# Optimization experiments

Hardware: AMD Instinct MI355X
Metric: run time of the kernel (lower is better)

Reference implementation:

```python
import jax, jax.numpy as jnp
import numpy as np
import math

B, S, D = 4, 2048, 1024


def setup_inputs() -> dict:
    key = jax.random.key(0)
    k1, k2, k3 = jax.random.split(key, 3)
    X = jax.random.normal(k1, (B, S, D), dtype=jnp.float32)
    # causal mask, broadcast over batch (True = keep)
    mask = jnp.broadcast_to(jnp.tril(jnp.ones((S, S), dtype=bool)), (B, S, S))
    # torch nn.Linear weights: y = x @ W.T; init scale ~ 1/sqrt(D)
    WQK = jax.random.normal(k2, (D, D), dtype=jnp.float32) / math.sqrt(D)
    WOV = jax.random.normal(k3, (D, D), dtype=jnp.float32) / math.sqrt(D)
    return {"X": X, "mask": mask, "WQK": WQK, "WOV": WOV}


def reference(X, mask, WQK, WOV):
    d = X.shape[-1]
    Q = jnp.einsum('bsd,ed->bse', X, WQK)          # WQK(X) = X @ WQK.T
    Sc = jnp.einsum('bse,bte->bst', Q, X)          # shared-QK scores: Q @ X^T
    # NOTE: original multiplies by sqrt(d_model) (not divide) - faithful
    Sc = Sc * jnp.asarray(math.sqrt(d), Sc.dtype)
    Sc = jnp.where(mask, Sc, -jnp.inf)
    A = jax.nn.softmax(Sc, axis=-1)                # dropout p=0.0 -> identity
    V = jnp.einsum('bsd,ed->bse', X, WOV)          # WOV(X)
    Y = jnp.einsum('bst,bte->bse', A, V)
    return (X + Y, A)
```

## Files before the change

### kernel.cpp

```cpp
#include <hip/hip_runtime.h>
#include <hip/hip_fp16.h>
#include <math.h>

typedef _Float16 half_t;
typedef _Float16 h8_t __attribute__((ext_vector_type(8)));
typedef _Float16 h4_t __attribute__((ext_vector_type(4)));
typedef float f4_t __attribute__((ext_vector_type(4)));

#define MFMA16(a, b, c) __builtin_amdgcn_mfma_f32_16x16x32_f16(a, b, c, 0, 0, 0)

static constexpr int kB = 4;
static constexpr int kS = 2048;
static constexpr int kD = 1024;
static constexpr int BM = 128;
static constexpr int BN = 128;
static constexpr int BK = 32;

__device__ __forceinline__ void gload16(const half_t* g, half_t* l) {
  __builtin_amdgcn_global_load_lds(
      (const __attribute__((address_space(1))) void*)g,
      (__attribute__((address_space(3))) void*)l, 16, 0, 0);
}

__device__ __forceinline__ void stage_tile(half_t* __restrict__ sm,
                                           const half_t* __restrict__ g, int ld) {
  const int t = threadIdx.x;
  const int r = t >> 2;
  const int c = (t & 3) * 8;
  gload16(&g[(size_t)r * ld + c], &sm[r * BK + c]);
  gload16(&g[(size_t)(r + 64) * ld + c], &sm[(r + 64) * BK + c]);
}

template <bool SPLIT>
__device__ __forceinline__ void stage_all(half_t* buf, const half_t* Ahi,
                                          const half_t* Alo, int lda,
                                          const half_t* Bhi, const half_t* Blo,
                                          int ldb, size_t ko) {
  stage_tile(buf, Ahi + ko, lda);
  stage_tile(buf + BM * BK, Bhi + ko, ldb);
  if (SPLIT) {
    stage_tile(buf + 2 * BM * BK, Alo + ko, lda);
    stage_tile(buf + 3 * BM * BK, Blo + ko, ldb);
  }
}

template <bool SPLIT>
__device__ __forceinline__ void gemm_core(const half_t* __restrict__ Ahi,
                                          const half_t* __restrict__ Alo, int lda,
                                          const half_t* __restrict__ Bhi,
                                          const half_t* __restrict__ Blo, int ldb,
                                          int k_iters, half_t* sm, f4_t acc[4][4]) {
  constexpr int BUFSZ = (SPLIT ? 4 : 2) * BM * BK;
  const int lane = threadIdx.x & 63;
  const int wid = threadIdx.x >> 6;
  const int wm = (wid >> 1) * 64;
  const int wn = (wid & 1) * 64;
  const int fr = lane & 15;
  const int fk = (lane >> 4) * 8;

  half_t* cur = sm;
  half_t* nxt = sm + BUFSZ;

  stage_all<SPLIT>(cur, Ahi, Alo, lda, Bhi, Blo, ldb, 0);
  asm volatile("s_waitcnt vmcnt(0)" ::: "memory");
  __builtin_amdgcn_s_barrier();

  for (int kk = 0; kk < k_iters; ++kk) {
    if (kk + 1 < k_iters)
      stage_all<SPLIT>(nxt, Ahi, Alo, lda, Bhi, Blo, ldb, (size_t)(kk + 1) * BK);
    const half_t* sAh = cur;
    const half_t* sBh = cur + BM * BK;
    const half_t* sAl = cur + 2 * BM * BK;
    const half_t* sBl = cur + 3 * BM * BK;
    h8_t a[4], b[4], al[4], bl[4];
#pragma unroll
    for (int i = 0; i < 4; ++i) {
      a[i] = *(const h8_t*)&sAh[(wm + i * 16 + fr) * BK + fk];
      b[i] = *(const h8_t*)&sBh[(wn + i * 16 + fr) * BK + fk];
      if (SPLIT) {
        al[i] = *(const h8_t*)&sAl[(wm + i * 16 + fr) * BK + fk];
        bl[i] = *(const h8_t*)&sBl[(wn + i * 16 + fr) * BK + fk];
      }
    }
#pragma unroll
    for (int i = 0; i < 4; ++i)
#pragma unroll
      for (int j = 0; j < 4; ++j) {
        acc[i][j] = MFMA16(a[i], b[j], acc[i][j]);
        if (SPLIT) {
          acc[i][j] = MFMA16(a[i], bl[j], acc[i][j]);
          acc[i][j] = MFMA16(al[i], b[j], acc[i][j]);
        }
      }
    asm volatile("s_waitcnt vmcnt(0)" ::: "memory");
    __builtin_amdgcn_s_barrier();
    half_t* t = cur; cur = nxt; nxt = t;
  }
}

__global__ __launch_bounds__(256) void gemm_q_kernel(
    const half_t* __restrict__ Xhi, const half_t* __restrict__ Xlo,
    const half_t* __restrict__ Whi, const half_t* __restrict__ Wlo,
    half_t* __restrict__ Qhi, half_t* __restrict__ Qlo) {
  __shared__ half_t sm[2 * 4 * BM * BK];
  const size_t arow = (size_t)blockIdx.y * BM;
  const size_t brow = (size_t)blockIdx.x * BN;
  f4_t acc[4][4] = {};
  gemm_core<true>(Xhi + arow * kD, Xlo + arow * kD, kD,
                  Whi + brow * kD, Wlo + brow * kD, kD, kD / BK, sm, acc);
  const int lane = threadIdx.x & 63;
  const int wid = threadIdx.x >> 6;
  const int wm = (wid >> 1) * 64, wn = (wid & 1) * 64;
  const int c16 = lane & 15, r4 = (lane >> 4) * 4;
#pragma unroll
  for (int i = 0; i < 4; ++i)
#pragma unroll
    for (int j = 0; j < 4; ++j)
#pragma unroll
      for (int r = 0; r < 4; ++r) {
        const size_t row = arow + wm + i * 16 + r4 + r;
        const size_t col = brow + wn + j * 16 + c16;
        const float q = acc[i][j][r];
        const half_t qh = (half_t)q;
        const half_t ql = (half_t)(q - (float)qh);
        const size_t idx = row * kD + col;
        Qhi[idx] = qh;
        Qlo[idx] = ql;
      }
}

__global__ __launch_bounds__(256) void gemm_v_kernel(
    const half_t* __restrict__ Xhi, const half_t* __restrict__ Whi,
    half_t* __restrict__ Vt) {
  __shared__ half_t sm[2 * 2 * BM * BK];
  const size_t arow = (size_t)blockIdx.y * BM;
  const size_t brow = (size_t)blockIdx.x * BN;
  f4_t acc[4][4] = {};
  gemm_core<false>(Xhi + arow * kD, nullptr, kD, Whi + brow * kD, nullptr, kD,
                   kD / BK, sm, acc);
  const int lane = threadIdx.x & 63;
  const int wid = threadIdx.x >> 6;
  const int wm = (wid >> 1) * 64, wn = (wid & 1) * 64;
  const int c16 = lane & 15, r4 = (lane >> 4) * 4;
#pragma unroll
  for (int i = 0; i < 4; ++i)
#pragma unroll
    for (int j = 0; j < 4; ++j)
#pragma unroll
      for (int r = 0; r < 4; ++r) {
        const size_t row = arow + wm + i * 16 + r4 + r;
        const size_t col = brow + wn + j * 16 + c16;
        const size_t bi = row >> 11;
        const size_t s = row & 2047;
        Vt[bi * (size_t)kD * kS + col * kS + s] = (half_t)acc[i][j][r];
      }
}

__global__ __launch_bounds__(256) void gemm_score_kernel(
    const half_t* __restrict__ Qhi, const half_t* __restrict__ Qlo,
    const half_t* __restrict__ Xhi, const half_t* __restrict__ Xlo,
    float* __restrict__ Sc) {
  const int tn = blockIdx.x, tm = blockIdx.y, bi = blockIdx.z;
  if (tn > tm) return;
  __shared__ half_t sm[2 * 4 * BM * BK];
  const size_t arow = (size_t)bi * kS + (size_t)tm * BM;
  const size_t brow = (size_t)bi * kS + (size_t)tn * BN;
  f4_t acc[4][4] = {};
  gemm_core<true>(Qhi + arow * kD, Qlo + arow * kD, kD,
                  Xhi + brow * kD, Xlo + brow * kD, kD, kD / BK, sm, acc);
  float* out = Sc + (size_t)bi * kS * kS;
  const int lane = threadIdx.x & 63;
  const int wid = threadIdx.x >> 6;
  const int wm = (wid >> 1) * 64, wn = (wid & 1) * 64;
  const int c16 = lane & 15, r4 = (lane >> 4) * 4;
#pragma unroll
  for (int i = 0; i < 4; ++i)
#pragma unroll
    for (int j = 0; j < 4; ++j)
#pragma unroll
      for (int r = 0; r < 4; ++r) {
        const int row = tm * BM + wm + i * 16 + r4 + r;
        const int col = tn * BN + wn + j * 16 + c16;
        out[(size_t)row * kS + col] = 32.0f * acc[i][j][r];
      }
}

__global__ __launch_bounds__(256) void softmax_kernel(float* __restrict__ A,
                                                      half_t* __restrict__ Ah) {
  const int rgl = blockIdx.x;
  const int s = rgl & 2047;
  float* row = A + (size_t)rgl * kS;
  half_t* hrow = Ah + (size_t)rgl * kS;
  const int tid = threadIdx.x;
  const int n = s + 1;
  float v[8];
  float mx = -INFINITY;
#pragma unroll
  for (int i = 0; i < 8; ++i) {
    const int t = tid + i * 256;
    v[i] = (t < n) ? row[t] : -INFINITY;
    mx = fmaxf(mx, v[i]);
  }
  for (int off = 32; off; off >>= 1) mx = fmaxf(mx, __shfl_xor(mx, off));
  __shared__ float red[8];
  const int lane = tid & 63, wid = tid >> 6;
  if (lane == 0) red[wid] = mx;
  __syncthreads();
  if (tid == 0) {
    float m = fmaxf(fmaxf(red[0], red[1]), fmaxf(red[2], red[3]));
    red[4] = m;
  }
  __syncthreads();
  mx = red[4];
  float sum = 0.0f;
#pragma unroll
  for (int i = 0; i < 8; ++i) {
    v[i] = (tid + i * 256 < n) ? __expf(v[i] - mx) : 0.0f;
    sum += v[i];
  }
  for (int off = 32; off; off >>= 1) sum += __shfl_xor(sum, off);
  __syncthreads();
  if (lane == 0) red[wid] = sum;
  __syncthreads();
  if (tid == 0) red[5] = 1.0f / (red[0] + red[1] + red[2] + red[3]);
  __syncthreads();
  const float inv = red[5];
#pragma unroll
  for (int i = 0; i < 8; ++i) {
    const int t = tid + i * 256;
    const float a = v[i] * inv;
    row[t] = a;
    hrow[t] = (half_t)a;
  }
}

__global__ __launch_bounds__(256) void gemm_y_kernel(
    const half_t* __restrict__ Ah, const half_t* __restrict__ Vt,
    const float* __restrict__ X, float* __restrict__ Out) {
  __shared__ half_t sm[2 * 2 * BM * BK];
  const int tn = blockIdx.x, bi = blockIdx.z;
  const int tm = (kS / BM - 1) - blockIdx.y;
  const size_t abase = ((size_t)bi * kS + (size_t)tm * BM) * kS;
  const size_t bbase = ((size_t)bi * kD + (size_t)tn * BN) * kS;
  f4_t acc[4][4] = {};
  gemm_core<false>(Ah + abase, nullptr, kS, Vt + bbase, nullptr, kS,
                   (tm + 1) * BM / BK, sm, acc);
  const size_t obase = (size_t)bi * kS * kD;
  const int lane = threadIdx.x & 63;
  const int wid = threadIdx.x >> 6;
  const int wm = (wid >> 1) * 64, wn = (wid & 1) * 64;
  const int c16 = lane & 15, r4 = (lane >> 4) * 4;
#pragma unroll
  for (int i = 0; i < 4; ++i)
#pragma unroll
    for (int j = 0; j < 4; ++j)
#pragma unroll
      for (int r = 0; r < 4; ++r) {
        const size_t row = (size_t)tm * BM + wm + i * 16 + r4 + r;
        const size_t col = (size_t)tn * BN + wn + j * 16 + c16;
        const size_t idx = obase + row * kD + col;
        Out[idx] = X[idx] + acc[i][j][r];
      }
}

__global__ __launch_bounds__(256) void split_kernel(const float* __restrict__ x,
                                                    half_t* __restrict__ hi,
                                                    half_t* __restrict__ lo, int n4) {
  const int i = blockIdx.x * 256 + threadIdx.x;
  if (i >= n4) return;
  const float4 v = ((const float4*)x)[i];
  const float vv[4] = {v.x, v.y, v.z, v.w};
  h4_t h, l;
#pragma unroll
  for (int j = 0; j < 4; ++j) {
    const half_t hh = (half_t)vv[j];
    h[j] = hh;
    l[j] = (half_t)(vv[j] - (float)hh);
  }
  ((h4_t*)hi)[i] = h;
  ((h4_t*)lo)[i] = l;
}

__global__ __launch_bounds__(256) void cvt_kernel(const float* __restrict__ x,
                                                  half_t* __restrict__ hi, int n4) {
  const int i = blockIdx.x * 256 + threadIdx.x;
  if (i >= n4) return;
  const float4 v = ((const float4*)x)[i];
  h4_t h;
  h[0] = (half_t)v.x; h[1] = (half_t)v.y; h[2] = (half_t)v.z; h[3] = (half_t)v.w;
  ((h4_t*)hi)[i] = h;
}

extern "C" void kernel_launch(void* const* d_in, const int* in_sizes, int n_in,
                              void* d_out, int out_size, void* d_ws, size_t ws_size,
                              hipStream_t stream) {
  const float* X   = (const float*)d_in[0];
  const float* WQK = (const float*)d_in[2];
  const float* WOV = (const float*)d_in[3];

  constexpr size_t nX = (size_t)kB * kS * kD;
  constexpr size_t nW = (size_t)kD * kD;
  constexpr size_t nA = (size_t)kB * kS * kS;

  float* out0 = (float*)d_out;
  float* outA = out0 + nX;

  half_t* ws = (half_t*)d_ws;
  half_t* Xhi = ws; ws += nX;
  half_t* Xlo = ws; ws += nX;
  half_t* Qhi = ws; ws += nX;
  half_t* Qlo = ws; ws += nX;
  half_t* Whi = ws; ws += nW;
  half_t* Wlo = ws; ws += nW;
  half_t* WVh = ws; ws += nW;
  half_t* Vt  = ws; ws += nX;
  half_t* Ah  = ws; ws += nA;
  const size_t need_bytes = (size_t)((char*)ws - (char*)d_ws);
  if (ws_size < need_bytes) return;

  split_kernel<<<(int)(nX / 4 / 256), 256, 0, stream>>>(X, Xhi, Xlo, (int)(nX / 4));
  split_kernel<<<(int)(nW / 4 / 256), 256, 0, stream>>>(WQK, Whi, Wlo, (int)(nW / 4));
  cvt_kernel<<<(int)(nW / 4 / 256), 256, 0, stream>>>(WOV, WVh, (int)(nW / 4));

  gemm_q_kernel<<<dim3(kD / BN, kB * kS / BM), 256, 0, stream>>>(Xhi, Xlo, Whi, Wlo, Qhi, Qlo);
  gemm_v_kernel<<<dim3(kD / BN, kB * kS / BM), 256, 0, stream>>>(Xhi, WVh, Vt);
  gemm_score_kernel<<<dim3(kS / BN, kS / BM, kB), 256, 0, stream>>>(Qhi, Qlo, Xhi, Xlo, outA);
  softmax_kernel<<<kB * kS, 256, 0, stream>>>(outA, Ah);
  gemm_y_kernel<<<dim3(kD / BN, kS / BM, kB), 256, 0, stream>>>(Ah, Vt, X, out0);
}
```

Before: 391.5 us.

## Use 512-thread blocks with 8 waves and XOR-swizzled LDS tiles in GEMMs

Doubles the GEMM block size to 512 threads (8 waves arranged 2x4, each computing a 64x32 sub-tile) so each wave holds half as many accumulators, and each thread stages one 16-byte chunk per tile instead of two. It also applies an XOR swizzle on the k-column of global loads and on the fragment reads, intended to reduce LDS bank conflicts. The aim is more waves in flight to hide latency, at the cost of less register-level reuse per wave and more LDS traffic per MFMA.

```diff
diff --git a/kernel.cpp b/kernel.cpp
--- a/kernel.cpp
+++ b/kernel.cpp
@@ -15,6 +15,7 @@
 static constexpr int BM = 128;
 static constexpr int BN = 128;
 static constexpr int BK = 32;
+static constexpr int NT = 512;
 
 __device__ __forceinline__ void gload16(const half_t* g, half_t* l) {
   __builtin_amdgcn_global_load_lds(
@@ -26,9 +27,8 @@
                                            const half_t* __restrict__ g, int ld) {
   const int t = threadIdx.x;
   const int r = t >> 2;
-  const int c = (t & 3) * 8;
-  gload16(&g[(size_t)r * ld + c], &sm[r * BK + c]);
-  gload16(&g[(size_t)(r + 64) * ld + c], &sm[(r + 64) * BK + c]);
+  const int c = ((t & 3) * 8) ^ ((((r >> 1) & 3)) << 3);
+  gload16(&g[(size_t)r * ld + c], &sm[r * BK + (t & 3) * 8]);
 }
 
 template <bool SPLIT>
@@ -49,14 +49,14 @@
                                           const half_t* __restrict__ Alo, int lda,
                                           const half_t* __restrict__ Bhi,
                                           const half_t* __restrict__ Blo, int ldb,
-                                          int k_iters, half_t* sm, f4_t acc[4][4]) {
+                                          int k_iters, half_t* sm, f4_t acc[4][2]) {
   constexpr int BUFSZ = (SPLIT ? 4 : 2) * BM * BK;
   const int lane = threadIdx.x & 63;
   const int wid = threadIdx.x >> 6;
-  const int wm = (wid >> 1) * 64;
-  const int wn = (wid & 1) * 64;
+  const int wm = (wid >> 2) * 64;
+  const int wn = (wid & 3) * 32;
   const int fr = lane & 15;
-  const int fk = (lane >> 4) * 8;
+  const int fk = (((lane >> 4) * 8) ^ (((lane >> 1) & 3) << 3));
 
   half_t* cur = sm;
   half_t* nxt = sm + BUFSZ;
@@ -72,20 +72,21 @@
     const half_t* sBh = cur + BM * BK;
     const half_t* sAl = cur + 2 * BM * BK;
     const half_t* sBl = cur + 3 * BM * BK;
-    h8_t a[4], b[4], al[4], bl[4];
+    h8_t a[4], b[2], al[4], bl[2];
 #pragma unroll
     for (int i = 0; i < 4; ++i) {
       a[i] = *(const h8_t*)&sAh[(wm + i * 16 + fr) * BK + fk];
-      b[i] = *(const h8_t*)&sBh[(wn + i * 16 + fr) * BK + fk];
-      if (SPLIT) {
-        al[i] = *(const h8_t*)&sAl[(wm + i * 16 + fr) * BK + fk];
-        bl[i] = *(const h8_t*)&sBl[(wn + i * 16 + fr) * BK + fk];
-      }
+      if (SPLIT) al[i] = *(const h8_t*)&sAl[(wm + i * 16 + fr) * BK + fk];
     }
 #pragma unroll
+    for (int j = 0; j < 2; ++j) {
+      b[j] = *(const h8_t*)&sBh[(wn + j * 16 + fr) * BK + fk];
+      if (SPLIT) bl[j] = *(const h8_t*)&sBl[(wn + j * 16 + fr) * BK + fk];
+    }
+#pragma unroll
     for (int i = 0; i < 4; ++i)
 #pragma unroll
-      for (int j = 0; j < 4; ++j) {
+      for (int j = 0; j < 2; ++j) {
         acc[i][j] = MFMA16(a[i], b[j], acc[i][j]);
         if (SPLIT) {
           acc[i][j] = MFMA16(a[i], bl[j], acc[i][j]);
@@ -98,24 +99,24 @@
   }
 }
 
-__global__ __launch_bounds__(256) void gemm_q_kernel(
+__global__ __launch_bounds__(NT) void gemm_q_kernel(
     const half_t* __restrict__ Xhi, const half_t* __restrict__ Xlo,
     const half_t* __restrict__ Whi, const half_t* __restrict__ Wlo,
     half_t* __restrict__ Qhi, half_t* __restrict__ Qlo) {
   __shared__ half_t sm[2 * 4 * BM * BK];
   const size_t arow = (size_t)blockIdx.y * BM;
   const size_t brow = (size_t)blockIdx.x * BN;
-  f4_t acc[4][4] = {};
+  f4_t acc[4][2] = {};
   gemm_core<true>(Xhi + arow * kD, Xlo + arow * kD, kD,
                   Whi + brow * kD, Wlo + brow * kD, kD, kD / BK, sm, acc);
   const int lane = threadIdx.x & 63;
   const int wid = threadIdx.x >> 6;
-  const int wm = (wid >> 1) * 64, wn = (wid & 1) * 64;
+  const int wm = (wid >> 2) * 64, wn = (wid & 3) * 32;
   const int c16 = lane & 15, r4 = (lane >> 4) * 4;
 #pragma unroll
   for (int i = 0; i < 4; ++i)
 #pragma unroll
-    for (int j = 0; j < 4; ++j)
+    for (int j = 0; j < 2; ++j)
 #pragma unroll
       for (int r = 0; r < 4; ++r) {
         const size_t row = arow + wm + i * 16 + r4 + r;
@@ -129,23 +130,23 @@
       }
 }
 
-__global__ __launch_bounds__(256) void gemm_v_kernel(
+__global__ __launch_bounds__(NT) void gemm_v_kernel(
     const half_t* __restrict__ Xhi, const half_t* __restrict__ Whi,
     half_t* __restrict__ Vt) {
   __shared__ half_t sm[2 * 2 * BM * BK];
   const size_t arow = (size_t)blockIdx.y * BM;
   const size_t brow = (size_t)blockIdx.x * BN;
-  f4_t acc[4][4] = {};
+  f4_t acc[4][2] = {};
   gemm_core<false>(Xhi + arow * kD, nullptr, kD, Whi + brow * kD, nullptr, kD,
                    kD / BK, sm, acc);
   const int lane = threadIdx.x & 63;
   const int wid = threadIdx.x >> 6;
-  const int wm = (wid >> 1) * 64, wn = (wid & 1) * 64;
+  const int wm = (wid >> 2) * 64, wn = (wid & 3) * 32;
   const int c16 = lane & 15, r4 = (lane >> 4) * 4;
 #pragma unroll
   for (int i = 0; i < 4; ++i)
 #pragma unroll
-    for (int j = 0; j < 4; ++j)
+    for (int j = 0; j < 2; ++j)
 #pragma unroll
       for (int r = 0; r < 4; ++r) {
         const size_t row = arow + wm + i * 16 + r4 + r;
@@ -156,7 +157,7 @@
       }
 }
 
-__global__ __launch_bounds__(256) void gemm_score_kernel(
+__global__ __launch_bounds__(NT) void gemm_score_kernel(
     const half_t* __restrict__ Qhi, const half_t* __restrict__ Qlo,
     const half_t* __restrict__ Xhi, const half_t* __restrict__ Xlo,
     float* __restrict__ Sc) {
@@ -165,18 +166,18 @@
   __shared__ half_t sm[2 * 4 * BM * BK];
   const size_t arow = (size_t)bi * kS + (size_t)tm * BM;
   const size_t brow = (size_t)bi * kS + (size_t)tn * BN;
-  f4_t acc[4][4] = {};
+  f4_t acc[4][2] = {};
   gemm_core<true>(Qhi + arow * kD, Qlo + arow * kD, kD,
                   Xhi + brow * kD, Xlo + brow * kD, kD, kD / BK, sm, acc);
   float* out = Sc + (size_t)bi * kS * kS;
   const int lane = threadIdx.x & 63;
   const int wid = threadIdx.x >> 6;
-  const int wm = (wid >> 1) * 64, wn = (wid & 1) * 64;
+  const int wm = (wid >> 2) * 64, wn = (wid & 3) * 32;
   const int c16 = lane & 15, r4 = (lane >> 4) * 4;
 #pragma unroll
   for (int i = 0; i < 4; ++i)
 #pragma unroll
-    for (int j = 0; j < 4; ++j)
+    for (int j = 0; j < 2; ++j)
 #pragma unroll
       for (int r = 0; r < 4; ++r) {
         const int row = tm * BM + wm + i * 16 + r4 + r;
@@ -234,7 +235,7 @@
   }
 }
 
-__global__ __launch_bounds__(256) void gemm_y_kernel(
+__global__ __launch_bounds__(NT) void gemm_y_kernel(
     const half_t* __restrict__ Ah, const half_t* __restrict__ Vt,
     const float* __restrict__ X, float* __restrict__ Out) {
   __shared__ half_t sm[2 * 2 * BM * BK];
@@ -242,18 +243,18 @@
   const int tm = (kS / BM - 1) - blockIdx.y;
   const size_t abase = ((size_t)bi * kS + (size_t)tm * BM) * kS;
   const size_t bbase = ((size_t)bi * kD + (size_t)tn * BN) * kS;
-  f4_t acc[4][4] = {};
+  f4_t acc[4][2] = {};
   gemm_core<false>(Ah + abase, nullptr, kS, Vt + bbase, nullptr, kS,
                    (tm + 1) * BM / BK, sm, acc);
   const size_t obase = (size_t)bi * kS * kD;
   const int lane = threadIdx.x & 63;
   const int wid = threadIdx.x >> 6;
-  const int wm = (wid >> 1) * 64, wn = (wid & 1) * 64;
+  const int wm = (wid >> 2) * 64, wn = (wid & 3) * 32;
   const int c16 = lane & 15, r4 = (lane >> 4) * 4;
 #pragma unroll
   for (int i = 0; i < 4; ++i)
 #pragma unroll
-    for (int j = 0; j < 4; ++j)
+    for (int j = 0; j < 2; ++j)
 #pragma unroll
       for (int r = 0; r < 4; ++r) {
         const size_t row = (size_t)tm * BM + wm + i * 16 + r4 + r;
@@ -322,9 +323,9 @@
   split_kernel<<<(int)(nW / 4 / 256), 256, 0, stream>>>(WQK, Whi, Wlo, (int)(nW / 4));
   cvt_kernel<<<(int)(nW / 4 / 256), 256, 0, stream>>>(WOV, WVh, (int)(nW / 4));
 
-  gemm_q_kernel<<<dim3(kD / BN, kB * kS / BM), 256, 0, stream>>>(Xhi, Xlo, Whi, Wlo, Qhi, Qlo);
-  gemm_v_kernel<<<dim3(kD / BN, kB * kS / BM), 256, 0, stream>>>(Xhi, WVh, Vt);
-  gemm_score_kernel<<<dim3(kS / BN, kS / BM, kB), 256, 0, stream>>>(Qhi, Qlo, Xhi, Xlo, outA);
+  gemm_q_kernel<<<dim3(kD / BN, kB * kS / BM), NT, 0, stream>>>(Xhi, Xlo, Whi, Wlo, Qhi, Qlo);
+  gemm_v_kernel<<<dim3(kD / BN, kB * kS / BM), NT, 0, stream>>>(Xhi, WVh, Vt);
+  gemm_score_kernel<<<dim3(kS / BN, kS / BM, kB), NT, 0, stream>>>(Qhi, Qlo, Xhi, Xlo, outA);
   softmax_kernel<<<kB * kS, 256, 0, stream>>>(outA, Ah);
-  gemm_y_kernel<<<dim3(kD / BN, kS / BM, kB), 256, 0, stream>>>(Ah, Vt, X, out0);
-}
+  gemm_y_kernel<<<dim3(kD / BN, kS / BM, kB), NT, 0, stream>>>(Ah, Vt, X, out0);
+}
```

Result: faster. 380.0 us (-2.9%).
